# Optimization experiments

Hardware: AMD Instinct MI355X
Metric: run time of the kernel (lower is better)

The kernel has to match this reference:

```python
import jax, jax.numpy as jnp
import numpy as np

EPS = 1e-5  # torch BatchNorm1d default eps

def spmm(rows, cols, vals, x, n_rows):
    # COO sparse [n_rows, n_cols] @ dense x [n_cols, d] via gather + segment_sum
    return jax.ops.segment_sum(vals[:, None] * x[cols], rows, num_segments=n_rows)

def linear_bn_relu(x, Wl, b, g, beta):
    h = x @ Wl.T + b
    mu = jnp.mean(h, axis=0)
    var = jnp.mean((h - mu) ** 2, axis=0)  # biased var, as torch BN training mode
    return jax.nn.relu((h - mu) * jax.lax.rsqrt(var + EPS) * g + beta)

def setup_inputs() -> dict:
    key = jax.random.key(0)
    ks = jax.random.split(key, 20)
    NQ, NI, NT, D, OUT = 8192, 8192, 4096, 256, 128
    EQI, EIT = 262144, 131072
    inp = {
        'feature_q': jax.random.normal(ks[0], (NQ, D), jnp.float32),
        'feature_i': jax.random.normal(ks[1], (NI, D), jnp.float32),
        'feature_t': jax.random.normal(ks[2], (NT, D), jnp.float32),
        'qi_src': jax.random.randint(ks[3], (EQI,), 0, NQ, jnp.int32),
        'qi_dst': jax.random.randint(ks[4], (EQI,), 0, NI, jnp.int32),
        'qi_val': jax.random.uniform(ks[5], (EQI,), jnp.float32),
        'it_src': jax.random.randint(ks[6], (EIT,), 0, NI, jnp.int32),
        'it_dst': jax.random.randint(ks[7], (EIT,), 0, NT, jnp.int32),
        'it_val': jax.random.uniform(ks[8], (EIT,), jnp.float32),
        'W': jax.random.normal(ks[9], (D, D), jnp.float32) * np.sqrt(2.0 / D),
        'Wq': jax.random.normal(ks[10], (OUT, 2 * D), jnp.float32) * 0.02,
        'bq': jnp.zeros((OUT,), jnp.float32),
        'gq': jnp.ones((OUT,), jnp.float32),
        'betaq': jnp.zeros((OUT,), jnp.float32),
        'Wi': jax.random.normal(ks[11], (OUT, 2 * D), jnp.float32) * 0.02,
        'bi': jnp.zeros((OUT,), jnp.float32),
        'gi': jnp.ones((OUT,), jnp.float32),
        'betai': jnp.zeros((OUT,), jnp.float32),
        'Wt': jax.random.normal(ks[12], (OUT, 2 * D), jnp.float32) * 0.02,
        'bt': jnp.zeros((OUT,), jnp.float32),
        'gt': jnp.ones((OUT,), jnp.float32),
        'betat': jnp.zeros((OUT,), jnp.float32),
        'Q': jax.random.normal(ks[13], (OUT, OUT), jnp.float32) * (1.0 / np.sqrt(OUT)),
    }
    return inp

def reference(feature_q, feature_i, feature_t, qi_src, qi_dst, qi_val,
              it_src, it_dst, it_val, W, Wq, bq, gq, betaq,
              Wi, bi, gi, betai, Wt, bt, gt, betat, Q):
    NQ, NI, NT = feature_q.shape[0], feature_i.shape[0], feature_t.shape[0]
    # drop_out = 0.0 -> sparse_drop is identity with scale 1/(1-0)=1
    hq_in = feature_i @ W  # [NI, H]
    hidden_q = jax.nn.relu(spmm(qi_src, qi_dst, qi_val, hq_in, NQ))
    hi_from_q = spmm(qi_dst, qi_src, qi_val, feature_q @ W, NI)  # M_qi.T @ (fq W)
    hi_from_t = spmm(it_src, it_dst, it_val, feature_t @ W, NI)  # M_it @ (ft W)
    hidden_i = jax.nn.relu(hi_from_q + hi_from_t)
    hidden_t = jax.nn.relu(spmm(it_dst, it_src, it_val, feature_i @ W, NT))  # M_it.T
    embed_q = linear_bn_relu(jnp.concatenate([hidden_q, feature_q], axis=1), Wq, bq, gq, betaq)
    embed_i = linear_bn_relu(jnp.concatenate([hidden_i, feature_i], axis=1), Wi, bi, gi, betai)
    embed_t = linear_bn_relu(jnp.concatenate([hidden_t, feature_t], axis=1), Wt, bt, gt, betat)
    score_qi = (embed_q @ Q) @ embed_i.T
    score_it = (embed_i @ Q) @ embed_t.T
    return score_qi, score_it
```

## Files before the change

### kernel.cpp

```cpp
#include <hip/hip_runtime.h>
#include <stddef.h>
#include <stdint.h>

using u16 = unsigned short;
typedef __attribute__((ext_vector_type(8))) short short8;
typedef __attribute__((ext_vector_type(4))) float f32x4;

constexpr int NQ = 8192, NI = 8192, NTT = 4096, DIM = 256, DOUT = 128;
constexpr int EQI = 262144, EIT = 131072, EB = EQI + EIT;
constexpr float BN_EPS = 1e-5f;

constexpr size_t al(size_t x) { return (x + 255) & ~(size_t)255; }
constexpr size_t BO_FQW = 0;
constexpr size_t BO_FTW = BO_FQW + (size_t)NQ * DIM * 2;
constexpr size_t BO_FIW = al(BO_FTW + (size_t)NTT * DIM * 2);
constexpr size_t BO_CQ  = al(BO_FIW + (size_t)NI * DIM * 2);
constexpr size_t BO_CI  = al(BO_CQ + (size_t)NQ * 512 * 2);
constexpr size_t BO_CT  = al(BO_CI + (size_t)NI * 512 * 2);
constexpr size_t BO_LQ  = al(BO_CT + (size_t)NTT * 512 * 2);
constexpr size_t BO_LI  = al(BO_LQ + (size_t)NQ * DOUT * 4);
constexpr size_t BO_LT  = al(BO_LI + (size_t)NI * DOUT * 4);
constexpr size_t BO_EQB = al(BO_LT + (size_t)NTT * DOUT * 4);
constexpr size_t BO_EIB = al(BO_EQB + (size_t)NQ * DOUT * 2);
constexpr size_t BO_ETB = al(BO_EIB + (size_t)NI * DOUT * 2);
constexpr size_t BO_EQQ = al(BO_ETB + (size_t)NTT * DOUT * 2);
constexpr size_t BO_EIQ = al(BO_EQQ + (size_t)NQ * DOUT * 2);
constexpr size_t BO_WTR = al(BO_EIQ + (size_t)NI * DOUT * 2);
constexpr size_t BO_WXQ = al(BO_WTR + (size_t)DIM * DIM * 2);
constexpr size_t BO_WXI = al(BO_WXQ + (size_t)DOUT * 512 * 2);
constexpr size_t BO_WXT = al(BO_WXI + (size_t)DOUT * 512 * 2);
constexpr size_t BO_QTR = al(BO_WXT + (size_t)DOUT * 512 * 2);
constexpr size_t BO_STAT = al(BO_QTR + (size_t)DOUT * DOUT * 2);
constexpr size_t BO_AOFF = al(BO_STAT + 1024 * 4);
constexpr size_t BO_ACUR = al(BO_AOFF + (size_t)(NQ + 1) * 4);
constexpr size_t BO_ACOL = al(BO_ACUR + (size_t)NQ * 4);
constexpr size_t BO_AVAL = al(BO_ACOL + (size_t)EQI * 4);
constexpr size_t BO_BOFF = al(BO_AVAL + (size_t)EQI * 4);
constexpr size_t BO_BCUR = al(BO_BOFF + (size_t)(NI + 1) * 4);
constexpr size_t BO_BCOL = al(BO_BCUR + (size_t)NI * 4);
constexpr size_t BO_BVAL = al(BO_BCOL + (size_t)EB * 4);
constexpr size_t BO_DOFF = al(BO_BVAL + (size_t)EB * 4);
constexpr size_t BO_DCUR = al(BO_DOFF + (size_t)(NTT + 1) * 4);
constexpr size_t BO_DCOL = al(BO_DCUR + (size_t)NTT * 4);
constexpr size_t BO_DVAL = al(BO_DCOL + (size_t)EIT * 4);

__device__ __forceinline__ u16 f2bf(float f) {
    union { float f; uint32_t u; } v;
    v.f = f;
    uint32_t u = v.u;
    u += 0x7FFFu + ((u >> 16) & 1u);
    return (u16)(u >> 16);
}
__device__ __forceinline__ float bf2f(u16 h) {
    union { uint32_t u; float f; } v;
    v.u = (uint32_t)h << 16;
    return v.f;
}

__global__ __launch_bounds__(256) void hist4_kernel(const int* __restrict__ k0, int E0, int* c0,
                                                    const int* __restrict__ k1, int E1, int* c1,
                                                    const int* __restrict__ k2, int E2, int* c2,
                                                    const int* __restrict__ k3, int E3, int* c3) {
    int idx = blockIdx.x * 256 + threadIdx.x;
    if (idx < E0) { atomicAdd(&c0[k0[idx]], 1); return; }
    idx -= E0;
    if (idx < E1) { atomicAdd(&c1[k1[idx]], 1); return; }
    idx -= E1;
    if (idx < E2) { atomicAdd(&c2[k2[idx]], 1); return; }
    idx -= E2;
    if (idx < E3) atomicAdd(&c3[k3[idx]], 1);
}

__global__ __launch_bounds__(1024) void scan3_kernel(int* cA, int* oA, int* cB, int* oB,
                                                     int* cD, int* oD) {
    int* cnt; int* offs; int n;
    if (blockIdx.x == 0) { cnt = cA; offs = oA; n = NQ; }
    else if (blockIdx.x == 1) { cnt = cB; offs = oB; n = NI; }
    else { cnt = cD; offs = oD; n = NTT; }
    __shared__ int swv[16];
    __shared__ int s_carry;
    const int t = threadIdx.x;
    const int lane = t & 63, wv = t >> 6;
    if (t == 0) s_carry = 0;
    __syncthreads();
    for (int base = 0; base < n; base += 1024) {
        int v = (base + t < n) ? cnt[base + t] : 0;
        int x = v;
#pragma unroll
        for (int off = 1; off < 64; off <<= 1) {
            int y = __shfl_up(x, off, 64);
            if (lane >= off) x += y;
        }
        if (lane == 63) swv[wv] = x;
        __syncthreads();
        if (wv == 0 && lane < 16) {
            int ws = swv[lane];
#pragma unroll
            for (int off = 1; off < 16; off <<= 1) {
                int y = __shfl_up(ws, off, 16);
                if ((lane & 15) >= off) ws += y;
            }
            swv[lane] = ws;
        }
        __syncthreads();
        const int carry = s_carry;
        const int incl = carry + ((wv > 0) ? swv[wv - 1] : 0) + x;
        if (base + t < n) {
            offs[base + t] = incl - v;
            cnt[base + t] = incl - v;
        }
        __syncthreads();
        if (t == 1023) s_carry = incl;
        __syncthreads();
    }
    if (t == 0) offs[n] = s_carry;
}

struct Scat {
    const int* key; const int* oth; const float* val;
    int E, coff;
    int* cur; int* col; float* sv;
};
struct ScatDesc { Scat s0, s1, s2, s3; };

__global__ __launch_bounds__(256) void scatter4_kernel(ScatDesc d) {
    int idx = blockIdx.x * 256 + threadIdx.x;
    Scat sg;
    if (idx < d.s0.E) sg = d.s0;
    else if ((idx -= d.s0.E) < d.s1.E) sg = d.s1;
    else if ((idx -= d.s1.E) < d.s2.E) sg = d.s2;
    else if ((idx -= d.s2.E) < d.s3.E) sg = d.s3;
    else return;
    int p = atomicAdd(&sg.cur[sg.key[idx]], 1);
    sg.col[p] = sg.oth[idx] + sg.coff;
    sg.sv[p] = sg.val[idx];
}

__global__ __launch_bounds__(256) void spmm3_kernel(
    const int* __restrict__ offs0, const int* __restrict__ cols0, const float* __restrict__ vals0,
    const u16* __restrict__ X0, u16* __restrict__ Y0, int nb0,
    const int* __restrict__ offs1, const int* __restrict__ cols1, const float* __restrict__ vals1,
    const u16* __restrict__ X1, u16* __restrict__ Y1, int nb1,
    const int* __restrict__ offs2, const int* __restrict__ cols2, const float* __restrict__ vals2,
    const u16* __restrict__ X2, u16* __restrict__ Y2) {
    int b = blockIdx.x;
    const int* offs; const int* cols; const float* vals; const u16* X; u16* Y;
    if (b < nb0) { offs = offs0; cols = cols0; vals = vals0; X = X0; Y = Y0; }
    else if ((b -= nb0) < nb1) { offs = offs1; cols = cols1; vals = vals1; X = X1; Y = Y1; }
    else { b -= nb1; offs = offs2; cols = cols2; vals = vals2; X = X2; Y = Y2; }
    const int w = threadIdx.x >> 6, lane = threadIdx.x & 63;
    const int r = b * 4 + w;
    const int s = offs[r], e = offs[r + 1];
    const u16* Xl = X + lane * 4;
    float a0 = 0.f, a1 = 0.f, a2 = 0.f, a3 = 0.f;
    int j = s;
    for (; j + 4 <= e; j += 4) {
        const int c0 = cols[j], c1 = cols[j + 1], c2 = cols[j + 2], c3 = cols[j + 3];
        const float v0 = vals[j], v1 = vals[j + 1], v2 = vals[j + 2], v3 = vals[j + 3];
        const ushort4 x0 = *(const ushort4*)(Xl + (size_t)c0 * DIM);
        const ushort4 x1 = *(const ushort4*)(Xl + (size_t)c1 * DIM);
        const ushort4 x2 = *(const ushort4*)(Xl + (size_t)c2 * DIM);
        const ushort4 x3 = *(const ushort4*)(Xl + (size_t)c3 * DIM);
        a0 = fmaf(v0, bf2f(x0.x), a0); a1 = fmaf(v0, bf2f(x0.y), a1);
        a2 = fmaf(v0, bf2f(x0.z), a2); a3 = fmaf(v0, bf2f(x0.w), a3);
        a0 = fmaf(v1, bf2f(x1.x), a0); a1 = fmaf(v1, bf2f(x1.y), a1);
        a2 = fmaf(v1, bf2f(x1.z), a2); a3 = fmaf(v1, bf2f(x1.w), a3);
        a0 = fmaf(v2, bf2f(x2.x), a0); a1 = fmaf(v2, bf2f(x2.y), a1);
        a2 = fmaf(v2, bf2f(x2.z), a2); a3 = fmaf(v2, bf2f(x2.w), a3);
        a0 = fmaf(v3, bf2f(x3.x), a0); a1 = fmaf(v3, bf2f(x3.y), a1);
        a2 = fmaf(v3, bf2f(x3.z), a2); a3 = fmaf(v3, bf2f(x3.w), a3);
    }
    for (; j < e; j++) {
        const int c = cols[j];
        const float v = vals[j];
        const ushort4 x = *(const ushort4*)(Xl + (size_t)c * DIM);
        a0 = fmaf(v, bf2f(x.x), a0); a1 = fmaf(v, bf2f(x.y), a1);
        a2 = fmaf(v, bf2f(x.z), a2); a3 = fmaf(v, bf2f(x.w), a3);
    }
    ushort4 o;
    o.x = f2bf(fmaxf(a0, 0.f)); o.y = f2bf(fmaxf(a1, 0.f));
    o.z = f2bf(fmaxf(a2, 0.f)); o.w = f2bf(fmaxf(a3, 0.f));
    *(ushort4*)(Y + (size_t)r * 512 + lane * 4) = o;
}

__global__ __launch_bounds__(256) void cvt_feat3_kernel(const float* __restrict__ fq,
                                                        const float* __restrict__ fi,
                                                        const float* __restrict__ ft,
                                                        u16* __restrict__ cq, u16* __restrict__ ci,
                                                        u16* __restrict__ ct) {
    int idx = blockIdx.x * 256 + threadIdx.x;
    const float* src; u16* dst;
    if (idx < NQ * 64) { src = fq; dst = cq; }
    else if ((idx -= NQ * 64) < NI * 64) { src = fi; dst = ci; }
    else { idx -= NI * 64; src = ft; dst = ct; }
    const float4 v = *(const float4*)(src + (size_t)idx * 4);
    const int r = idx >> 6, c = (idx & 63) * 4;
    ushort4 o;
    o.x = f2bf(v.x); o.y = f2bf(v.y); o.z = f2bf(v.z); o.w = f2bf(v.w);
    *(ushort4*)(dst + (size_t)r * 512 + 256 + c) = o;
}

__global__ __launch_bounds__(256) void cvt_weights_kernel(
    const float* __restrict__ W, u16* __restrict__ WTR, const float* __restrict__ Qm,
    u16* __restrict__ QTR, const float* __restrict__ Wq, u16* __restrict__ WXQ,
    const float* __restrict__ Wi, u16* __restrict__ WXI, const float* __restrict__ Wt,
    u16* __restrict__ WXT) {
    int idx = blockIdx.x * 256 + threadIdx.x;
    if (idx < DIM * DIM) {
        int n = idx >> 8, k = idx & 255;
        WTR[idx] = f2bf(W[(size_t)k * DIM + n]);
        return;
    }
    idx -= DIM * DIM;
    if (idx < DOUT * DOUT) {
        int n = idx >> 7, k = idx & 127;
        QTR[idx] = f2bf(Qm[(size_t)k * DOUT + n]);
        return;
    }
    idx -= DOUT * DOUT;
    if (idx < DOUT * 512) { WXQ[idx] = f2bf(Wq[idx]); return; }
    idx -= DOUT * 512;
    if (idx < DOUT * 512) { WXI[idx] = f2bf(Wi[idx]); return; }
    idx -= DOUT * 512;
    if (idx < DOUT * 512) WXT[idx] = f2bf(Wt[idx]);
}

template <int OUT_BF16>
__global__ __launch_bounds__(256) void gemm_bf16_nt_seg(
    const u16* __restrict__ A0, const u16* __restrict__ A1, const u16* __restrict__ A2,
    const u16* __restrict__ B0, const u16* __restrict__ B1, const u16* __restrict__ B2,
    void* __restrict__ C0, void* __restrict__ C1, void* __restrict__ C2,
    int ldc0, int ldc1, int ldc2, int yb0, int yb1, int xb0, int xb1, int xb2,
    int K, int lda, int ldb) {
    const int by = blockIdx.y, bx = blockIdx.x;
    const u16* A; const u16* B; void* Cout; int ldc; int xb; int byl;
    if (by < yb0) { A = A0; B = B0; Cout = C0; ldc = ldc0; xb = xb0; byl = by; }
    else if (by < yb0 + yb1) { A = A1; B = B1; Cout = C1; ldc = ldc1; xb = xb1; byl = by - yb0; }
    else { A = A2; B = B2; Cout = C2; ldc = ldc2; xb = xb2; byl = by - yb0 - yb1; }
    if (bx >= xb) return;

    __shared__ alignas(16) u16 As[128 * 64];
    __shared__ alignas(16) u16 Bs[128 * 64];
    const int tid = threadIdx.x;
    const int l = tid & 63;
    const int w = tid >> 6;
    const size_t m0 = (size_t)byl * 128;
    const size_t n0 = (size_t)bx * 128;
    const int lr = l >> 3;
    const int skb = ((l & 7) - lr) & 7;
    const u16* Ag = A + (m0 + (size_t)(w * 32 + lr)) * lda + skb * 8;
    const u16* Bg = B + (n0 + (size_t)(w * 32 + lr)) * ldb + skb * 8;
    u16* ldsA = As + (w * 32) * 64;
    u16* ldsB = Bs + (w * 32) * 64;

    const int fr = l & 15;
    const int fq = l >> 4;
    const int wmr = (w >> 1) * 64;
    const int wnr = (w & 1) * 64;

    f32x4 acc[4][4] = {};

    for (int k0 = 0; k0 < K; k0 += 64) {
#pragma unroll
        for (int t = 0; t < 4; t++) {
            __builtin_amdgcn_global_load_lds(
                (const __attribute__((address_space(1))) void*)(Ag + (size_t)t * 8 * lda + k0),
                (__attribute__((address_space(3))) void*)(ldsA + t * 8 * 64), 16, 0, 0);
            __builtin_amdgcn_global_load_lds(
                (const __attribute__((address_space(1))) void*)(Bg + (size_t)t * 8 * ldb + k0),
                (__attribute__((address_space(3))) void*)(ldsB + t * 8 * 64), 16, 0, 0);
        }
        __syncthreads();
#pragma unroll
        for (int ks = 0; ks < 2; ks++) {
            const int kb = ks * 4 + fq;
            short8 af[4], bf[4];
#pragma unroll
            for (int mt = 0; mt < 4; mt++) {
                const int r = wmr + mt * 16 + fr;
                af[mt] = *(const short8*)(As + r * 64 + ((kb + r) & 7) * 8);
            }
#pragma unroll
            for (int nt = 0; nt < 4; nt++) {
                const int r = wnr + nt * 16 + fr;
                bf[nt] = *(const short8*)(Bs + r * 64 + ((kb + r) & 7) * 8);
            }
#pragma unroll
            for (int mt = 0; mt < 4; mt++)
#pragma unroll
                for (int nt = 0; nt < 4; nt++)
                    acc[mt][nt] = __builtin_amdgcn_mfma_f32_16x16x32_bf16(af[mt], bf[nt],
                                                                          acc[mt][nt], 0, 0, 0);
        }
        __syncthreads();
    }
    const size_t crow = m0 + wmr + fq * 4;
    const size_t ccol = n0 + wnr + fr;
#pragma unroll
    for (int mt = 0; mt < 4; mt++)
#pragma unroll
        for (int nt = 0; nt < 4; nt++)
#pragma unroll
            for (int i = 0; i < 4; i++) {
                size_t r = crow + mt * 16 + i;
                size_t c = ccol + nt * 16;
                if (OUT_BF16)
                    ((u16*)Cout)[r * ldc + c] = f2bf(acc[mt][nt][i]);
                else
                    ((float*)Cout)[r * ldc + c] = acc[mt][nt][i];
            }
}

__global__ __launch_bounds__(256) void bn_stats3_kernel(const float* __restrict__ LQ,
                                                        const float* __restrict__ LI,
                                                        const float* __restrict__ LT,
                                                        float* __restrict__ STAT) {
    const float* h; int N; float* st;
    if (blockIdx.y == 0) { h = LQ; N = NQ; st = STAT; }
    else if (blockIdx.y == 1) { h = LI; N = NI; st = STAT + 256; }
    else { h = LT; N = NTT; st = STAT + 512; }
    const int t = threadIdx.x;
    const int c = t & 127, half = t >> 7;
    const int rows = N / gridDim.x;
    const int r0 = blockIdx.x * rows;
    float s = 0.f, ss = 0.f;
    for (int r = r0 + half; r < r0 + rows; r += 2) {
        float v = h[(size_t)r * DOUT + c];
        s += v;
        ss += v * v;
    }
    __shared__ float buf[256];
    buf[t] = s;
    __syncthreads();
    if (half == 0) s += buf[t + 128];
    __syncthreads();
    buf[t] = ss;
    __syncthreads();
    if (half == 0) {
        ss += buf[t + 128];
        atomicAdd(&st[c], s);
        atomicAdd(&st[DOUT + c], ss);
    }
}

__global__ __launch_bounds__(256) void bn_apply3_kernel(
    const float* __restrict__ LQ, const float* __restrict__ LI, const float* __restrict__ LT,
    const float* __restrict__ STAT, const float* __restrict__ gq, const float* __restrict__ bq,
    const float* __restrict__ gi, const float* __restrict__ bi, const float* __restrict__ gt,
    const float* __restrict__ bt, u16* __restrict__ EQB, u16* __restrict__ EIB,
    u16* __restrict__ ETB) {
    size_t idx = (size_t)blockIdx.x * 256 + threadIdx.x;
    const float* h; const float* st; const float* g; const float* be; u16* o; int N;
    if (idx < (size_t)NQ * DOUT) { h = LQ; st = STAT; g = gq; be = bq; o = EQB; N = NQ; }
    else if ((idx -= (size_t)NQ * DOUT) < (size_t)NI * DOUT) {
        h = LI; st = STAT + 256; g = gi; be = bi; o = EIB; N = NI;
    } else {
        idx -= (size_t)NI * DOUT;
        h = LT; st = STAT + 512; g = gt; be = bt; o = ETB; N = NTT;
    }
    const int c = (int)(idx & (DOUT - 1));
    const float inv_n = 1.0f / (float)N;
    const float mu = st[c] * inv_n;
    const float var = st[DOUT + c] * inv_n - mu * mu;
    float v = (h[idx] - mu) * rsqrtf(var + BN_EPS) * g[c] + be[c];
    o[idx] = f2bf(fmaxf(v, 0.f));
}

extern "C" void kernel_launch(void* const* d_in, const int* in_sizes, int n_in, void* d_out,
                              int out_size, void* d_ws, size_t ws_size, hipStream_t stream) {
    const float* feature_q = (const float*)d_in[0];
    const float* feature_i = (const float*)d_in[1];
    const float* feature_t = (const float*)d_in[2];
    const int* qi_src = (const int*)d_in[3];
    const int* qi_dst = (const int*)d_in[4];
    const float* qi_val = (const float*)d_in[5];
    const int* it_src = (const int*)d_in[6];
    const int* it_dst = (const int*)d_in[7];
    const float* it_val = (const float*)d_in[8];
    const float* W = (const float*)d_in[9];
    const float* Wq = (const float*)d_in[10];
    const float* gq = (const float*)d_in[12];
    const float* betaq = (const float*)d_in[13];
    const float* Wi = (const float*)d_in[14];
    const float* gi = (const float*)d_in[16];
    const float* betai = (const float*)d_in[17];
    const float* Wt = (const float*)d_in[18];
    const float* gt = (const float*)d_in[20];
    const float* betat = (const float*)d_in[21];
    const float* Qm = (const float*)d_in[22];
    float* out = (float*)d_out;
    char* ws = (char*)d_ws;

    u16* FQW = (u16*)(ws + BO_FQW);
    u16* FIW = (u16*)(ws + BO_FIW);
    u16* FTW = (u16*)(ws + BO_FTW);
    u16* CQ = (u16*)(ws + BO_CQ);
    u16* CI = (u16*)(ws + BO_CI);
    u16* CT = (u16*)(ws + BO_CT);
    float* LQ = (float*)(ws + BO_LQ);
    float* LI = (float*)(ws + BO_LI);
    float* LT = (float*)(ws + BO_LT);
    u16* EQB = (u16*)(ws + BO_EQB);
    u16* EIB = (u16*)(ws + BO_EIB);
    u16* ETB = (u16*)(ws + BO_ETB);
    u16* EQQ = (u16*)(ws + BO_EQQ);
    u16* EIQ = (u16*)(ws + BO_EIQ);
    u16* WTR = (u16*)(ws + BO_WTR);
    u16* WXQ = (u16*)(ws + BO_WXQ);
    u16* WXI = (u16*)(ws + BO_WXI);
    u16* WXT = (u16*)(ws + BO_WXT);
    u16* QTR = (u16*)(ws + BO_QTR);
    float* STAT = (float*)(ws + BO_STAT);
    int* Aoff = (int*)(ws + BO_AOFF); int* Acur = (int*)(ws + BO_ACUR);
    int* Acol = (int*)(ws + BO_ACOL); float* Aval = (float*)(ws + BO_AVAL);
    int* Boff = (int*)(ws + BO_BOFF); int* Bcur = (int*)(ws + BO_BCUR);
    int* Bcol = (int*)(ws + BO_BCOL); float* Bval = (float*)(ws + BO_BVAL);
    int* Doff = (int*)(ws + BO_DOFF); int* Dcur = (int*)(ws + BO_DCUR);
    int* Dcol = (int*)(ws + BO_DCOL); float* Dval = (float*)(ws + BO_DVAL);

    hipMemsetAsync(Acur, 0, NQ * sizeof(int), stream);
    hipMemsetAsync(Bcur, 0, NI * sizeof(int), stream);
    hipMemsetAsync(Dcur, 0, NTT * sizeof(int), stream);
    hipMemsetAsync(STAT, 0, 768 * sizeof(float), stream);

    cvt_feat3_kernel<<<(NQ + NI + NTT) * 64 / 256, 256, 0, stream>>>(feature_q, feature_i,
                                                                     feature_t, CQ, CI, CT);
    cvt_weights_kernel<<<(DIM * DIM + DOUT * DOUT + 3 * DOUT * 512 + 255) / 256, 256, 0, stream>>>(
        W, WTR, Qm, QTR, Wq, WXQ, Wi, WXI, Wt, WXT);

    hist4_kernel<<<(2 * EQI + 2 * EIT) / 256, 256, 0, stream>>>(qi_src, EQI, Acur, qi_dst, EQI,
                                                                Bcur, it_src, EIT, Bcur, it_dst,
                                                                EIT, Dcur);
    scan3_kernel<<<3, 1024, 0, stream>>>(Acur, Aoff, Bcur, Boff, Dcur, Doff);
    {
        ScatDesc d;
        d.s0 = {qi_src, qi_dst, qi_val, EQI, 0, Acur, Acol, Aval};
        d.s1 = {qi_dst, qi_src, qi_val, EQI, 0, Bcur, Bcol, Bval};
        d.s2 = {it_src, it_dst, it_val, EIT, NQ, Bcur, Bcol, Bval};
        d.s3 = {it_dst, it_src, it_val, EIT, 0, Dcur, Dcol, Dval};
        scatter4_kernel<<<(2 * EQI + 2 * EIT) / 256, 256, 0, stream>>>(d);
    }

    gemm_bf16_nt_seg<1><<<dim3(2, NQ / 128 + NI / 128 + NTT / 128), 256, 0, stream>>>(
        CQ + 256, CI + 256, CT + 256, WTR, WTR, WTR, FQW, FIW, FTW, DIM, DIM, DIM, NQ / 128,
        NI / 128, 2, 2, 2, DIM, 512, 256);

    spmm3_kernel<<<NQ / 4 + NI / 4 + NTT / 4, 256, 0, stream>>>(
        Aoff, Acol, Aval, FIW, CQ, NQ / 4, Boff, Bcol, Bval, FQW, CI, NI / 4, Doff, Dcol, Dval,
        FIW, CT);

    gemm_bf16_nt_seg<0><<<dim3(1, NQ / 128 + NI / 128 + NTT / 128), 256, 0, stream>>>(
        CQ, CI, CT, WXQ, WXI, WXT, LQ, LI, LT, DOUT, DOUT, DOUT, NQ / 128, NI / 128, 1, 1, 1, 512,
        512, 512);

    bn_stats3_kernel<<<dim3(32, 3), 256, 0, stream>>>(LQ, LI, LT, STAT);
    bn_apply3_kernel<<<((NQ + NI + NTT) * DOUT) / 256, 256, 0, stream>>>(
        LQ, LI, LT, STAT, gq, betaq, gi, betai, gt, betat, EQB, EIB, ETB);

    gemm_bf16_nt_seg<1><<<dim3(1, NQ / 128 + NI / 128), 256, 0, stream>>>(
        EQB, EIB, EIB, QTR, QTR, QTR, EQQ, EIQ, EIQ, DOUT, DOUT, DOUT, NQ / 128, NI / 128, 1, 1, 1,
        DOUT, DOUT, DOUT);

    gemm_bf16_nt_seg<0><<<dim3(NI / 128, NQ / 128 + NI / 128), 256, 0, stream>>>(
        EQQ, EIQ, EIQ, EIB, ETB, ETB, out, out + (size_t)NQ * NI, out + (size_t)NQ * NI, NI, NTT,
        NTT, NQ / 128, NI / 128, NI / 128, NTT / 128, NTT / 128, DOUT, DOUT, DOUT);
}
```

Baseline: 673.1 us.

## Merge prep kernels, fuse scatter with projection GEMM, fold BN stats into GEMM

Folds feature/weight conversion and histogramming into one prep kernel, and runs the CSR scatter and the W projection GEMM in a single launch. It also computes BatchNorm sums inside the linear GEMM epilogue via LDS and global atomics, rewrites the scan as a single-pass per-thread 8-element scan, vectorizes bn_apply, and uses nontemporal stores for the large score output. The aim is to cut launch count, drop a separate stats pass, and reduce cache pollution from the big output. The cost is more float atomics, which make the BN sums order-dependent, plus larger LDS use in the scatter blocks.

Measured after the change: 646.1 us. 1.04x faster.

```diff
diff --git a/kernel.cpp b/kernel.cpp
--- a/kernel.cpp
+++ b/kernel.cpp
@@ -9,6 +9,11 @@
 constexpr int NQ = 8192, NI = 8192, NTT = 4096, DIM = 256, DOUT = 128;
 constexpr int EQI = 262144, EIT = 131072, EB = EQI + EIT;
 constexpr float BN_EPS = 1e-5f;
+
+constexpr int NB_CVT = (NQ + NI + NTT) * 64 / 256;
+constexpr int NB_W = (DIM * DIM + DOUT * DOUT + 3 * DOUT * 512) / 256;
+constexpr int NB_HIST = (2 * EQI + 2 * EIT) / 256;
+constexpr int NB_SCAT = (2 * EQI + 2 * EIT) / 256;
 
 constexpr size_t al(size_t x) { return (x + 255) & ~(size_t)255; }
 constexpr size_t BO_FQW = 0;
@@ -57,18 +62,60 @@
     return v.f;
 }
 
-__global__ __launch_bounds__(256) void hist4_kernel(const int* __restrict__ k0, int E0, int* c0,
-                                                    const int* __restrict__ k1, int E1, int* c1,
-                                                    const int* __restrict__ k2, int E2, int* c2,
-                                                    const int* __restrict__ k3, int E3, int* c3) {
-    int idx = blockIdx.x * 256 + threadIdx.x;
-    if (idx < E0) { atomicAdd(&c0[k0[idx]], 1); return; }
-    idx -= E0;
-    if (idx < E1) { atomicAdd(&c1[k1[idx]], 1); return; }
-    idx -= E1;
-    if (idx < E2) { atomicAdd(&c2[k2[idx]], 1); return; }
-    idx -= E2;
-    if (idx < E3) atomicAdd(&c3[k3[idx]], 1);
+__global__ __launch_bounds__(256) void prep_kernel(
+    const float* __restrict__ fq, const float* __restrict__ fi, const float* __restrict__ ft,
+    u16* __restrict__ cq, u16* __restrict__ ci, u16* __restrict__ ct,
+    const float* __restrict__ W, u16* __restrict__ WTR, const float* __restrict__ Qm,
+    u16* __restrict__ QTR, const float* __restrict__ Wq, u16* __restrict__ WXQ,
+    const float* __restrict__ Wi, u16* __restrict__ WXI, const float* __restrict__ Wt,
+    u16* __restrict__ WXT, const int* __restrict__ qi_src, const int* __restrict__ qi_dst,
+    const int* __restrict__ it_src, const int* __restrict__ it_dst, int* __restrict__ Acur,
+    int* __restrict__ Bcur, int* __restrict__ Dcur) {
+    int b = blockIdx.x;
+    if (b < NB_CVT) {
+        int idx = b * 256 + threadIdx.x;
+        const float* src; u16* dst;
+        if (idx < NQ * 64) { src = fq; dst = cq; }
+        else if ((idx -= NQ * 64) < NI * 64) { src = fi; dst = ci; }
+        else { idx -= NI * 64; src = ft; dst = ct; }
+        const float4 v = *(const float4*)(src + (size_t)idx * 4);
+        const int r = idx >> 6, c = (idx & 63) * 4;
+        ushort4 o;
+        o.x = f2bf(v.x); o.y = f2bf(v.y); o.z = f2bf(v.z); o.w = f2bf(v.w);
+        *(ushort4*)(dst + (size_t)r * 512 + 256 + c) = o;
+        return;
+    }
+    b -= NB_CVT;
+    if (b < NB_W) {
+        int idx = b * 256 + threadIdx.x;
+        if (idx < DIM * DIM) {
+            int n = idx >> 8, k = idx & 255;
+            WTR[idx] = f2bf(W[(size_t)k * DIM + n]);
+            return;
+        }
+        idx -= DIM * DIM;
+        if (idx < DOUT * DOUT) {
+            int n = idx >> 7, k = idx & 127;
+            QTR[idx] = f2bf(Qm[(size_t)k * DOUT + n]);
+            return;
+        }
+        idx -= DOUT * DOUT;
+        if (idx < DOUT * 512) { WXQ[idx] = f2bf(Wq[idx]); return; }
+        idx -= DOUT * 512;
+        if (idx < DOUT * 512) { WXI[idx] = f2bf(Wi[idx]); return; }
+        idx -= DOUT * 512;
+        WXT[idx] = f2bf(Wt[idx]);
+        return;
+    }
+    b -= NB_W;
+    int idx = b * 256 + threadIdx.x;
+    if (idx < EQI) { atomicAdd(&Acur[qi_src[idx]], 1); return; }
+    idx -= EQI;
+    if (idx < EQI) { atomicAdd(&Bcur[qi_dst[idx]], 1); return; }
+    idx -= EQI;
+    if (idx < EIT) { atomicAdd(&Bcur[it_src[idx]], 1); return; }
+    idx -= EIT;
+    atomicAdd(&Dcur[it_dst[idx]], 1);
 }
 
 __global__ __launch_bounds__(1024) void scan3_kernel(int* cA, int* oA, int* cB, int* oB,
@@ -78,42 +125,53 @@
     else if (blockIdx.x == 1) { cnt = cB; offs = oB; n = NI; }
     else { cnt = cD; offs = oD; n = NTT; }
     __shared__ int swv[16];
-    __shared__ int s_carry;
     const int t = threadIdx.x;
     const int lane = t & 63, wv = t >> 6;
-    if (t == 0) s_carry = 0;
+    const int base = t * 8;
+    int v[8];
+    int run = 0;
+    if (base + 8 <= n) {
+        const int4 p0 = *(const int4*)(cnt + base);
+        const int4 p1 = *(const int4*)(cnt + base + 4);
+        int tmp[8] = {p0.x, p0.y, p0.z, p0.w, p1.x, p1.y, p1.z, p1.w};
+#pragma unroll
+        for (int i = 0; i < 8; i++) { run += tmp[i]; v[i] = run; }
+    } else {
+#pragma unroll
+        for (int i = 0; i < 8; i++) {
+            int x = (base + i < n) ? cnt[base + i] : 0;
+            run += x;
+            v[i] = run;
+        }
+    }
+    int x = run;
+#pragma unroll
+    for (int off = 1; off < 64; off <<= 1) {
+        int y = __shfl_up(x, off, 64);
+        if (lane >= off) x += y;
+    }
+    if (lane == 63) swv[wv] = x;
     __syncthreads();
-    for (int base = 0; base < n; base += 1024) {
-        int v = (base + t < n) ? cnt[base + t] : 0;
-        int x = v;
-#pragma unroll
-        for (int off = 1; off < 64; off <<= 1) {
-            int y = __shfl_up(x, off, 64);
-            if (lane >= off) x += y;
-        }
-        if (lane == 63) swv[wv] = x;
-        __syncthreads();
-        if (wv == 0 && lane < 16) {
-            int ws = swv[lane];
-#pragma unroll
-            for (int off = 1; off < 16; off <<= 1) {
-                int y = __shfl_up(ws, off, 16);
-                if ((lane & 15) >= off) ws += y;
-            }
-            swv[lane] = ws;
-        }
-        __syncthreads();
-        const int carry = s_carry;
-        const int incl = carry + ((wv > 0) ? swv[wv - 1] : 0) + x;
-        if (base + t < n) {
-            offs[base + t] = incl - v;
-            cnt[base + t] = incl - v;
-        }
-        __syncthreads();
-        if (t == 1023) s_carry = incl;
-        __syncthreads();
-    }
-    if (t == 0) offs[n] = s_carry;
+    if (wv == 0 && lane < 16) {
+        int ws = swv[lane];
+#pragma unroll
+        for (int off = 1; off < 16; off <<= 1) {
+            int y = __shfl_up(ws, off, 16);
+            if (lane >= off) ws += y;
+        }
+        swv[lane] = ws;
+    }
+    __syncthreads();
+    const int tbase = ((wv > 0) ? swv[wv - 1] : 0) + (x - run);
+#pragma unroll
+    for (int i = 0; i < 8; i++) {
+        if (base + i < n) {
+            const int e = tbase + ((i > 0) ? v[i - 1] : 0);
+            offs[base + i] = e;
+            cnt[base + i] = e;
+        }
+    }
+    if (t == 0) offs[n] = swv[15];
 }
 
 struct Scat {
@@ -123,17 +181,157 @@
 };
 struct ScatDesc { Scat s0, s1, s2, s3; };
 
-__global__ __launch_bounds__(256) void scatter4_kernel(ScatDesc d) {
-    int idx = blockIdx.x * 256 + threadIdx.x;
-    Scat sg;
-    if (idx < d.s0.E) sg = d.s0;
-    else if ((idx -= d.s0.E) < d.s1.E) sg = d.s1;
-    else if ((idx -= d.s1.E) < d.s2.E) sg = d.s2;
-    else if ((idx -= d.s2.E) < d.s3.E) sg = d.s3;
-    else return;
-    int p = atomicAdd(&sg.cur[sg.key[idx]], 1);
-    sg.col[p] = sg.oth[idx] + sg.coff;
-    sg.sv[p] = sg.val[idx];
+template <int OUT_BF16, int FUSE_STATS, int NT_STORE>
+__device__ __forceinline__ void gemm_tile(const u16* __restrict__ A, const u16* __restrict__ B,
+                                          void* __restrict__ Cout, int ldc, int byl, int bx,
+                                          int K, int lda, int ldb, u16* As, u16* Bs,
+                                          float* __restrict__ stat) {
+    const int tid = threadIdx.x;
+    const int l = tid & 63;
+    const int w = tid >> 6;
+    const size_t m0 = (size_t)byl * 128;
+    const size_t n0 = (size_t)bx * 128;
+    const int lr = l >> 3;
+    const int skb = ((l & 7) - lr) & 7;
+    const u16* Ag = A + (m0 + (size_t)(w * 32 + lr)) * lda + skb * 8;
+    const u16* Bg = B + (n0 + (size_t)(w * 32 + lr)) * ldb + skb * 8;
+    u16* ldsA = As + (w * 32) * 64;
+    u16* ldsB = Bs + (w * 32) * 64;
+
+    const int fr = l & 15;
+    const int fq = l >> 4;
+    const int wmr = (w >> 1) * 64;
+    const int wnr = (w & 1) * 64;
+
+    f32x4 acc[4][4] = {};
+
+    for (int k0 = 0; k0 < K; k0 += 64) {
+#pragma unroll
+        for (int t = 0; t < 4; t++) {
+            __builtin_amdgcn_global_load_lds(
+                (const __attribute__((address_space(1))) void*)(Ag + (size_t)t * 8 * lda + k0),
+                (__attribute__((address_space(3))) void*)(ldsA + t * 8 * 64), 16, 0, 0);
+            __builtin_amdgcn_global_load_lds(
+                (const __attribute__((address_space(1))) void*)(Bg + (size_t)t * 8 * ldb + k0),
+                (__attribute__((address_space(3))) void*)(ldsB + t * 8 * 64), 16, 0, 0);
+        }
+        __syncthreads();
+#pragma unroll
+        for (int ks = 0; ks < 2; ks++) {
+            const int kb = ks * 4 + fq;
+            short8 af[4], bf[4];
+#pragma unroll
+            for (int mt = 0; mt < 4; mt++) {
+                const int r = wmr + mt * 16 + fr;
+                af[mt] = *(const short8*)(As + r * 64 + ((kb + r) & 7) * 8);
+            }
+#pragma unroll
+            for (int nt = 0; nt < 4; nt++) {
+                const int r = wnr + nt * 16 + fr;
+                bf[nt] = *(const short8*)(Bs + r * 64 + ((kb + r) & 7) * 8);
+            }
+#pragma unroll
+            for (int mt = 0; mt < 4; mt++)
+#pragma unroll
+                for (int nt = 0; nt < 4; nt++)
+                    acc[mt][nt] = __builtin_amdgcn_mfma_f32_16x16x32_bf16(af[mt], bf[nt],
+                                                                          acc[mt][nt], 0, 0, 0);
+        }
+        __syncthreads();
+    }
+
+    if constexpr (FUSE_STATS) {
+        float* csum = (float*)As;
+        ((float*)As)[tid] = 0.f;
+        __syncthreads();
+#pragma unroll
+        for (int nt = 0; nt < 4; nt++) {
+            float s = 0.f, ss = 0.f;
+#pragma unroll
+            for (int mt = 0; mt < 4; mt++)
+#pragma unroll
+                for (int i = 0; i < 4; i++) {
+                    const float vv = acc[mt][nt][i];
+                    s += vv;
+                    ss += vv * vv;
+                }
+            const int c = wnr + fr + nt * 16;
+            atomicAdd(&csum[c], s);
+            atomicAdd(&csum[DOUT + c], ss);
+        }
+        __syncthreads();
+        if (tid < DOUT) {
+            atomicAdd(&stat[tid], csum[tid]);
+            atomicAdd(&stat[DOUT + tid], csum[DOUT + tid]);
+        }
+    }
+
+    const size_t crow = m0 + wmr + fq * 4;
+    const size_t ccol = n0 + wnr + fr;
+#pragma unroll
+    for (int mt = 0; mt < 4; mt++)
+#pragma unroll
+        for (int nt = 0; nt < 4; nt++)
+#pragma unroll
+            for (int i = 0; i < 4; i++) {
+                const size_t r = crow + mt * 16 + i;
+                const size_t c = ccol + nt * 16;
+                if constexpr (OUT_BF16)
+                    ((u16*)Cout)[r * ldc + c] = f2bf(acc[mt][nt][i]);
+                else if constexpr (NT_STORE)
+                    __builtin_nontemporal_store(acc[mt][nt][i], &((float*)Cout)[r * ldc + c]);
+                else
+                    ((float*)Cout)[r * ldc + c] = acc[mt][nt][i];
+            }
+}
+
+__global__ __launch_bounds__(256) void scatter_proj_kernel(
+    ScatDesc d, const u16* __restrict__ CQh, const u16* __restrict__ CIh,
+    const u16* __restrict__ CTh, const u16* __restrict__ WTRp, u16* __restrict__ FQWp,
+    u16* __restrict__ FIWp, u16* __restrict__ FTWp) {
+    __shared__ alignas(16) u16 As[128 * 64];
+    __shared__ alignas(16) u16 Bs[128 * 64];
+    int b = blockIdx.x;
+    if (b < NB_SCAT) {
+        int idx = b * 256 + threadIdx.x;
+        Scat sg;
+        if (idx < d.s0.E) sg = d.s0;
+        else if ((idx -= d.s0.E) < d.s1.E) sg = d.s1;
+        else if ((idx -= d.s1.E) < d.s2.E) sg = d.s2;
+        else { idx -= d.s2.E; sg = d.s3; }
+        const int p = atomicAdd(&sg.cur[sg.key[idx]], 1);
+        sg.col[p] = sg.oth[idx] + sg.coff;
+        sg.sv[p] = sg.val[idx];
+        return;
+    }
+    const int g = b - NB_SCAT;
+    const int bx = g & 1, by = g >> 1;
+    const u16* A; u16* C; int byl;
+    if (by < NQ / 128) { A = CQh; C = FQWp; byl = by; }
+    else if (by < NQ / 128 + NI / 128) { A = CIh; C = FIWp; byl = by - NQ / 128; }
+    else { A = CTh; C = FTWp; byl = by - NQ / 128 - NI / 128; }
+    gemm_tile<1, 0, 0>(A, WTRp, C, DIM, byl, bx, DIM, 512, DIM, As, Bs, nullptr);
+}
+
+template <int OUT_BF16, int FUSE_STATS, int NT_STORE>
+__global__ __launch_bounds__(256) void gemm_seg_kernel(
+    const u16* __restrict__ A0, const u16* __restrict__ A1, const u16* __restrict__ A2,
+    const u16* __restrict__ B0, const u16* __restrict__ B1, const u16* __restrict__ B2,
+    void* __restrict__ C0, void* __restrict__ C1, void* __restrict__ C2,
+    int ldc0, int ldc1, int ldc2, int yb0, int yb1, int xb0, int xb1, int xb2,
+    int K, int lda, int ldb, float* st0, float* st1, float* st2) {
+    __shared__ alignas(16) u16 As[128 * 64];
+    __shared__ alignas(16) u16 Bs[128 * 64];
+    const int by = blockIdx.y, bx = blockIdx.x;
+    const u16* A; const u16* B; void* Cout; int ldc; int xb; int byl; float* st;
+    if (by < yb0) { A = A0; B = B0; Cout = C0; ldc = ldc0; xb = xb0; byl = by; st = st0; }
+    else if (by < yb0 + yb1) {
+        A = A1; B = B1; Cout = C1; ldc = ldc1; xb = xb1; byl = by - yb0; st = st1;
+    } else {
+        A = A2; B = B2; Cout = C2; ldc = ldc2; xb = xb2; byl = by - yb0 - yb1; st = st2;
+    }
+    if (bx >= xb) return;
+    gemm_tile<OUT_BF16, FUSE_STATS, NT_STORE>(A, B, Cout, ldc, byl, bx, K, lda, ldb, As, Bs, st);
 }
 
 __global__ __launch_bounds__(256) void spmm3_kernel(
@@ -183,187 +381,37 @@
     *(ushort4*)(Y + (size_t)r * 512 + lane * 4) = o;
 }
 
-__global__ __launch_bounds__(256) void cvt_feat3_kernel(const float* __restrict__ fq,
-                                                        const float* __restrict__ fi,
-                                                        const float* __restrict__ ft,
-                                                        u16* __restrict__ cq, u16* __restrict__ ci,
-                                                        u16* __restrict__ ct) {
-    int idx = blockIdx.x * 256 + threadIdx.x;
-    const float* src; u16* dst;
-    if (idx < NQ * 64) { src = fq; dst = cq; }
-    else if ((idx -= NQ * 64) < NI * 64) { src = fi; dst = ci; }
-    else { idx -= NI * 64; src = ft; dst = ct; }
-    const float4 v = *(const float4*)(src + (size_t)idx * 4);
-    const int r = idx >> 6, c = (idx & 63) * 4;
-    ushort4 o;
-    o.x = f2bf(v.x); o.y = f2bf(v.y); o.z = f2bf(v.z); o.w = f2bf(v.w);
-    *(ushort4*)(dst + (size_t)r * 512 + 256 + c) = o;
-}
-
-__global__ __launch_bounds__(256) void cvt_weights_kernel(
-    const float* __restrict__ W, u16* __restrict__ WTR, const float* __restrict__ Qm,
-    u16* __restrict__ QTR, const float* __restrict__ Wq, u16* __restrict__ WXQ,
-    const float* __restrict__ Wi, u16* __restrict__ WXI, const float* __restrict__ Wt,
-    u16* __restrict__ WXT) {
-    int idx = blockIdx.x * 256 + threadIdx.x;
-    if (idx < DIM * DIM) {
-        int n = idx >> 8, k = idx & 255;
-        WTR[idx] = f2bf(W[(size_t)k * DIM + n]);
-        return;
-    }
-    idx -= DIM * DIM;
-    if (idx < DOUT * DOUT) {
-        int n = idx >> 7, k = idx & 127;
-        QTR[idx] = f2bf(Qm[(size_t)k * DOUT + n]);
-        return;
-    }
-    idx -= DOUT * DOUT;
-    if (idx < DOUT * 512) { WXQ[idx] = f2bf(Wq[idx]); return; }
-    idx -= DOUT * 512;
-    if (idx < DOUT * 512) { WXI[idx] = f2bf(Wi[idx]); return; }
-    idx -= DOUT * 512;
-    if (idx < DOUT * 512) WXT[idx] = f2bf(Wt[idx]);
-}
-
-template <int OUT_BF16>
-__global__ __launch_bounds__(256) void gemm_bf16_nt_seg(
-    const u16* __restrict__ A0, const u16* __restrict__ A1, const u16* __restrict__ A2,
-    const u16* __restrict__ B0, const u16* __restrict__ B1, const u16* __restrict__ B2,
-    void* __restrict__ C0, void* __restrict__ C1, void* __restrict__ C2,
-    int ldc0, int ldc1, int ldc2, int yb0, int yb1, int xb0, int xb1, int xb2,
-    int K, int lda, int ldb) {
-    const int by = blockIdx.y, bx = blockIdx.x;
-    const u16* A; const u16* B; void* Cout; int ldc; int xb; int byl;
-    if (by < yb0) { A = A0; B = B0; Cout = C0; ldc = ldc0; xb = xb0; byl = by; }
-    else if (by < yb0 + yb1) { A = A1; B = B1; Cout = C1; ldc = ldc1; xb = xb1; byl = by - yb0; }
-    else { A = A2; B = B2; Cout = C2; ldc = ldc2; xb = xb2; byl = by - yb0 - yb1; }
-    if (bx >= xb) return;
-
-    __shared__ alignas(16) u16 As[128 * 64];
-    __shared__ alignas(16) u16 Bs[128 * 64];
-    const int tid = threadIdx.x;
-    const int l = tid & 63;
-    const int w = tid >> 6;
-    const size_t m0 = (size_t)byl * 128;
-    const size_t n0 = (size_t)bx * 128;
-    const int lr = l >> 3;
-    const int skb = ((l & 7) - lr) & 7;
-    const u16* Ag = A + (m0 + (size_t)(w * 32 + lr)) * lda + skb * 8;
-    const u16* Bg = B + (n0 + (size_t)(w * 32 + lr)) * ldb + skb * 8;
-    u16* ldsA = As + (w * 32) * 64;
-    u16* ldsB = Bs + (w * 32) * 64;
-
-    const int fr = l & 15;
-    const int fq = l >> 4;
-    const int wmr = (w >> 1) * 64;
-    const int wnr = (w & 1) * 64;
-
-    f32x4 acc[4][4] = {};
-
-    for (int k0 = 0; k0 < K; k0 += 64) {
-#pragma unroll
-        for (int t = 0; t < 4; t++) {
-            __builtin_amdgcn_global_load_lds(
-                (const __attribute__((address_space(1))) void*)(Ag + (size_t)t * 8 * lda + k0),
-                (__attribute__((address_space(3))) void*)(ldsA + t * 8 * 64), 16, 0, 0);
-            __builtin_amdgcn_global_load_lds(
-                (const __attribute__((address_space(1))) void*)(Bg + (size_t)t * 8 * ldb + k0),
-                (__attribute__((address_space(3))) void*)(ldsB + t * 8 * 64), 16, 0, 0);
-        }
-        __syncthreads();
-#pragma unroll
-        for (int ks = 0; ks < 2; ks++) {
-            const int kb = ks * 4 + fq;
-            short8 af[4], bf[4];
-#pragma unroll
-            for (int mt = 0; mt < 4; mt++) {
-                const int r = wmr + mt * 16 + fr;
-                af[mt] = *(const short8*)(As + r * 64 + ((kb + r) & 7) * 8);
-            }
-#pragma unroll
-            for (int nt = 0; nt < 4; nt++) {
-                const int r = wnr + nt * 16 + fr;
-                bf[nt] = *(const short8*)(Bs + r * 64 + ((kb + r) & 7) * 8);
-            }
-#pragma unroll
-            for (int mt = 0; mt < 4; mt++)
-#pragma unroll
-                for (int nt = 0; nt < 4; nt++)
-                    acc[mt][nt] = __builtin_amdgcn_mfma_f32_16x16x32_bf16(af[mt], bf[nt],
-                                                                          acc[mt][nt], 0, 0, 0);
-        }
-        __syncthreads();
-    }
-    const size_t crow = m0 + wmr + fq * 4;
-    const size_t ccol = n0 + wnr + fr;
-#pragma unroll
-    for (int mt = 0; mt < 4; mt++)
-#pragma unroll
-        for (int nt = 0; nt < 4; nt++)
-#pragma unroll
-            for (int i = 0; i < 4; i++) {
-                size_t r = crow + mt * 16 + i;
-                size_t c = ccol + nt * 16;
-                if (OUT_BF16)
-                    ((u16*)Cout)[r * ldc + c] = f2bf(acc[mt][nt][i]);
-                else
-                    ((float*)Cout)[r * ldc + c] = acc[mt][nt][i];
-            }
-}
-
-__global__ __launch_bounds__(256) void bn_stats3_kernel(const float* __restrict__ LQ,
-                                                        const float* __restrict__ LI,
-                                                        const float* __restrict__ LT,
-                                                        float* __restrict__ STAT) {
-    const float* h; int N; float* st;
-    if (blockIdx.y == 0) { h = LQ; N = NQ; st = STAT; }
-    else if (blockIdx.y == 1) { h = LI; N = NI; st = STAT + 256; }
-    else { h = LT; N = NTT; st = STAT + 512; }
-    const int t = threadIdx.x;
-    const int c = t & 127, half = t >> 7;
-    const int rows = N / gridDim.x;
-    const int r0 = blockIdx.x * rows;
-    float s = 0.f, ss = 0.f;
-    for (int r = r0 + half; r < r0 + rows; r += 2) {
-        float v = h[(size_t)r * DOUT + c];
-        s += v;
-        ss += v * v;
-    }
-    __shared__ float buf[256];
-    buf[t] = s;
-    __syncthreads();
-    if (half == 0) s += buf[t + 128];
-    __syncthreads();
-    buf[t] = ss;
-    __syncthreads();
-    if (half == 0) {
-        ss += buf[t + 128];
-        atomicAdd(&st[c], s);
-        atomicAdd(&st[DOUT + c], ss);
-    }
-}
-
 __global__ __launch_bounds__(256) void bn_apply3_kernel(
     const float* __restrict__ LQ, const float* __restrict__ LI, const float* __restrict__ LT,
     const float* __restrict__ STAT, const float* __restrict__ gq, const float* __restrict__ bq,
     const float* __restrict__ gi, const float* __restrict__ bi, const float* __restrict__ gt,
     const float* __restrict__ bt, u16* __restrict__ EQB, u16* __restrict__ EIB,
     u16* __restrict__ ETB) {
-    size_t idx = (size_t)blockIdx.x * 256 + threadIdx.x;
-    const float* h; const float* st; const float* g; const float* be; u16* o; int N;
-    if (idx < (size_t)NQ * DOUT) { h = LQ; st = STAT; g = gq; be = bq; o = EQB; N = NQ; }
-    else if ((idx -= (size_t)NQ * DOUT) < (size_t)NI * DOUT) {
-        h = LI; st = STAT + 256; g = gi; be = bi; o = EIB; N = NI;
+    size_t q4 = (size_t)blockIdx.x * 256 + threadIdx.x;
+    const float* h; const float* st; const float* g; const float* be; u16* o; float inv_n;
+    if (q4 < (size_t)NQ * 32) {
+        h = LQ; st = STAT; g = gq; be = bq; o = EQB; inv_n = 1.0f / NQ;
+    } else if ((q4 -= (size_t)NQ * 32) < (size_t)NI * 32) {
+        h = LI; st = STAT + 256; g = gi; be = bi; o = EIB; inv_n = 1.0f / NI;
     } else {
-        idx -= (size_t)NI * DOUT;
-        h = LT; st = STAT + 512; g = gt; be = bt; o = ETB; N = NTT;
-    }
-    const int c = (int)(idx & (DOUT - 1));
-    const float inv_n = 1.0f / (float)N;
-    const float mu = st[c] * inv_n;
-    const float var = st[DOUT + c] * inv_n - mu * mu;
-    float v = (h[idx] - mu) * rsqrtf(var + BN_EPS) * g[c] + be[c];
-    o[idx] = f2bf(fmaxf(v, 0.f));
+        q4 -= (size_t)NI * 32;
+        h = LT; st = STAT + 512; g = gt; be = bt; o = ETB; inv_n = 1.0f / NTT;
+    }
+    const float4 hv = *(const float4*)(h + q4 * 4);
+    const int c0 = (int)((q4 * 4) & (DOUT - 1));
+    const float r[4] = {hv.x, hv.y, hv.z, hv.w};
+    u16 ov[4];
+#pragma unroll
+    for (int j = 0; j < 4; j++) {
+        const int c = c0 + j;
+        const float mu = st[c] * inv_n;
+        const float var = st[DOUT + c] * inv_n - mu * mu;
+        const float val = (r[j] - mu) * rsqrtf(var + BN_EPS) * g[c] + be[c];
+        ov[j] = f2bf(fmaxf(val, 0.f));
+    }
+    ushort4 pk;
+    pk.x = ov[0]; pk.y = ov[1]; pk.z = ov[2]; pk.w = ov[3];
+    *(ushort4*)(o + q4 * 4) = pk;
 }
 
 extern "C" void kernel_launch(void* const* d_in, const int* in_sizes, int n_in, void* d_out,
@@ -423,45 +471,39 @@
     hipMemsetAsync(Dcur, 0, NTT * sizeof(int), stream);
     hipMemsetAsync(STAT, 0, 768 * sizeof(float), stream);
 
-    cvt_feat3_kernel<<<(NQ + NI + NTT) * 64 / 256, 256, 0, stream>>>(feature_q, feature_i,
-                                                                     feature_t, CQ, CI, CT);
-    cvt_weights_kernel<<<(DIM * DIM + DOUT * DOUT + 3 * DOUT * 512 + 255) / 256, 256, 0, stream>>>(
-        W, WTR, Qm, QTR, Wq, WXQ, Wi, WXI, Wt, WXT);
-
-    hist4_kernel<<<(2 * EQI + 2 * EIT) / 256, 256, 0, stream>>>(qi_src, EQI, Acur, qi_dst, EQI,
-                                                                Bcur, it_src, EIT, Bcur, it_dst,
-                                                                EIT, Dcur);
+    prep_kernel<<<NB_CVT + NB_W + NB_HIST, 256, 0, stream>>>(
+        feature_q, feature_i, feature_t, CQ, CI, CT, W, WTR, Qm, QTR, Wq, WXQ, Wi, WXI, Wt, WXT,
+        qi_src, qi_dst, it_src, it_dst, Acur, Bcur, Dcur);
+
     scan3_kernel<<<3, 1024, 0, stream>>>(Acur, Aoff, Bcur, Boff, Dcur, Doff);
+
     {
         ScatDesc d;
         d.s0 = {qi_src, qi_dst, qi_val, EQI, 0, Acur, Acol, Aval};
         d.s1 = {qi_dst, qi_src, qi_val, EQI, 0, Bcur, Bcol, Bval};
         d.s2 = {it_src, it_dst, it_val, EIT, NQ, Bcur, Bcol, Bval};
         d.s3 = {it_dst, it_src, it_val, EIT, 0, Dcur, Dcol, Dval};
-        scatter4_kernel<<<(2 * EQI + 2 * EIT) / 256, 256, 0, stream>>>(d);
-    }
-
-    gemm_bf16_nt_seg<1><<<dim3(2, NQ / 128 + NI / 128 + NTT / 128), 256, 0, stream>>>(
-        CQ + 256, CI + 256, CT + 256, WTR, WTR, WTR, FQW, FIW, FTW, DIM, DIM, DIM, NQ / 128,
-        NI / 128, 2, 2, 2, DIM, 512, 256);
+        scatter_proj_kernel<<<NB_SCAT + 2 * (NQ / 128 + NI / 128 + NTT / 128), 256, 0, stream>>>(
+            d, CQ + 256, CI + 256, CT + 256, WTR, FQW, FIW, FTW);
+    }
 
     spmm3_kernel<<<NQ / 4 + NI / 4 + NTT / 4, 256, 0, stream>>>(
         Aoff, Acol, Aval, FIW, CQ, NQ / 4, Boff, Bcol, Bval, FQW, CI, NI / 4, Doff, Dcol, Dval,
         FIW, CT);
 
-    gemm_bf16_nt_seg<0><<<dim3(1, NQ / 128 + NI / 128 + NTT / 128), 256, 0, stream>>>(
+    gemm_seg_kernel<0, 1, 0><<<dim3(1, NQ / 128 + NI / 128 + NTT / 128), 256, 0, stream>>>(
         CQ, CI, CT, WXQ, WXI, WXT, LQ, LI, LT, DOUT, DOUT, DOUT, NQ / 128, NI / 128, 1, 1, 1, 512,
-        512, 512);
-
-    bn_stats3_kernel<<<dim3(32, 3), 256, 0, stream>>>(LQ, LI, LT, STAT);
-    bn_apply3_kernel<<<((NQ + NI + NTT) * DOUT) / 256, 256, 0, stream>>>(
+        512, 512, STAT, STAT + 256, STAT + 512);
+
+    bn_apply3_kernel<<<((NQ + NI + NTT) * 32) / 256, 256, 0, stream>>>(
         LQ, LI, LT, STAT, gq, betaq, gi, betai, gt, betat, EQB, EIB, ETB);
 
-    gemm_bf16_nt_seg<1><<<dim3(1, NQ / 128 + NI / 128), 256, 0, stream>>>(
+    gemm_seg_kernel<1, 0, 0><<<dim3(1, NQ / 128 + NI / 128), 256, 0, stream>>>(
         EQB, EIB, EIB, QTR, QTR, QTR, EQQ, EIQ, EIQ, DOUT, DOUT, DOUT, NQ / 128, NI / 128, 1, 1, 1,
-        DOUT, DOUT, DOUT);
-
-    gemm_bf16_nt_seg<0><<<dim3(NI / 128, NQ / 128 + NI / 128), 256, 0, stream>>>(
+        DOUT, DOUT, DOUT, nullptr, nullptr, nullptr);
+
+    gemm_seg_kernel<0, 0, 1><<<dim3(NI / 128, NQ / 128 + NI / 128), 256, 0, stream>>>(
         EQQ, EIQ, EIQ, EIB, ETB, ETB, out, out + (size_t)NQ * NI, out + (size_t)NQ * NI, NI, NTT,
-        NTT, NQ / 128, NI / 128, NI / 128, NTT / 128, NTT / 128, DOUT, DOUT, DOUT);
-}
+        NTT, NQ / 128, NI / 128, NI / 128, NTT / 128, NTT / 128, DOUT, DOUT, DOUT, nullptr,
+        nullptr, nullptr);
+}
```
